# Kernel optimization log

Hardware: AMD Instinct MI355X
Metric: run time of the kernel (lower is better)

The kernel has to match this reference:

```python
import jax, jax.numpy as jnp
import numpy as np

B, L, H, E, V, Z, T = 256, 2, 1024, 256, 28, 1024, 512
SOS_IDX, EOS_IDX = 1, 0


def setup_inputs() -> dict:
    key = jax.random.key(0)
    ks = jax.random.split(key, 16)
    s = 0.05
    emb = s * jax.random.normal(ks[0], (V, E), jnp.float32)
    emb = emb.at[EOS_IDX].set(0.0)  # padding_idx=0
    return {
        "z": jax.random.normal(ks[1], (B, Z), jnp.float32),
        "emb": emb,
        "w_zh": s * jax.random.normal(ks[2], (L * H, Z), jnp.float32),
        "b_zh": jnp.zeros((L * H,), jnp.float32),
        "w_ih0": s * jax.random.normal(ks[3], (3 * H, E), jnp.float32),
        "w_hh0": s * jax.random.normal(ks[4], (3 * H, H), jnp.float32),
        "b_ih0": jnp.zeros((3 * H,), jnp.float32),
        "b_hh0": jnp.zeros((3 * H,), jnp.float32),
        "w_ih1": s * jax.random.normal(ks[5], (3 * H, H), jnp.float32),
        "w_hh1": s * jax.random.normal(ks[6], (3 * H, H), jnp.float32),
        "b_ih1": jnp.zeros((3 * H,), jnp.float32),
        "b_hh1": jnp.zeros((3 * H,), jnp.float32),
        "w_out": s * jax.random.normal(ks[7], (V, H), jnp.float32),
        "b_out": jnp.zeros((V,), jnp.float32),
    }


def _gru_cell(x, h, w_ih, w_hh, b_ih, b_hh):
    # PyTorch GRU cell math
    gi = x @ w_ih.T + b_ih          # [B, 3H]
    gh = h @ w_hh.T + b_hh          # [B, 3H]
    i_r, i_z, i_n = jnp.split(gi, 3, axis=-1)
    h_r, h_z, h_n = jnp.split(gh, 3, axis=-1)
    r = jax.nn.sigmoid(i_r + h_r)
    zg = jax.nn.sigmoid(i_z + h_z)
    n = jnp.tanh(i_n + r * h_n)
    return (1.0 - zg) * n + zg * h


def reference(z, emb, w_zh, b_zh, w_ih0, w_hh0, b_ih0, b_hh0,
              w_ih1, w_hh1, b_ih1, b_hh1, w_out, b_out):
    # init hidden from latent: (B, L*H) -> per-layer (B, H)
    h = jnp.tanh(z @ w_zh.T + b_zh).reshape(-1, L, H)
    h0, h1 = h[:, 0, :], h[:, 1, :]
    tok0 = jnp.full((z.shape[0],), SOS_IDX, jnp.int32)
    keys = jax.random.split(jax.random.key(42), T)

    def step(carry, k):
        tok, h0, h1 = carry
        x = emb[tok]                         # [B, E] embedding lookup
        h0n = _gru_cell(x, h0, w_ih0, w_hh0, b_ih0, b_hh0)
        h1n = _gru_cell(h0n, h1, w_ih1, w_hh1, b_ih1, b_hh1)
        logit = h1n @ w_out.T + b_out        # [B, V]
        tok_n = jax.random.categorical(k, logit)  # multinomial(softmax(logit))
        return (tok_n, h0n, h1n), (logit, tok_n)

    _, (logits, tokens) = jax.lax.scan(step, (tok0, h0, h1), keys)
    # [T, B, V] -> [B, T, V]; [T, B] -> [B, T]
    return logits.transpose(1, 0, 2), tokens.T
```

## Files before the change

kernel.cpp:

```cpp
#include <hip/hip_runtime.h>

#define BB 256
#define HH 1024
#define EE 256
#define VV 28
#define ZZ 1024
#define TT 512
#define G3 3072
#define NTHR 256
#define TOKBASE (BB * TT * VV)

#define BM 64
#define BN 64
#define KT 32

#define MMN 48
#define NBN 64

typedef float f4 __attribute__((ext_vector_type(4)));
typedef float f32x4 __attribute__((ext_vector_type(4)));
typedef _Float16 f16x8 __attribute__((ext_vector_type(8)));
typedef unsigned short u16x4 __attribute__((ext_vector_type(4)));
typedef unsigned short u16x8 __attribute__((ext_vector_type(8)));

#define RES_SCALE 512.0f
#define INV_RES (1.0f / 512.0f)

__device__ __align__(16) float g_h0[2][BB][HH];
__device__ __align__(16) float g_h1[2][BB][HH];
__device__ __align__(16) float g_gh0b[BB][G3];
__device__ __align__(16) float g_gh1b[BB][G3];
__device__ __align__(16) float g_gi1[BB][G3];
__device__ __align__(16) float g_P0[VV][G3];
__device__ __align__(16) unsigned short g_h0t[32][2][4][BB][8];
__device__ __align__(16) unsigned short g_h1t[32][2][4][BB][8];
__device__ __align__(16) unsigned short g_wt[3][NBN][32][2][4][MMN][8];

__device__ __forceinline__ uint2 tf2x32(unsigned k0, unsigned k1,
                                        unsigned x0, unsigned x1) {
  unsigned ks2 = k0 ^ k1 ^ 0x1BD11BDAu;
  unsigned ksl[3] = {k0, k1, ks2};
  x0 += k0; x1 += k1;
#pragma unroll
  for (int g = 0; g < 5; ++g) {
    const int r0 = (g & 1) ? 17 : 13;
    const int r1 = (g & 1) ? 29 : 15;
    const int r2 = (g & 1) ? 16 : 26;
    const int r3 = (g & 1) ? 24 : 6;
    x0 += x1; x1 = (x1 << r0) | (x1 >> (32 - r0)); x1 ^= x0;
    x0 += x1; x1 = (x1 << r1) | (x1 >> (32 - r1)); x1 ^= x0;
    x0 += x1; x1 = (x1 << r2) | (x1 >> (32 - r2)); x1 ^= x0;
    x0 += x1; x1 = (x1 << r3) | (x1 >> (32 - r3)); x1 ^= x0;
    x0 += ksl[(g + 1) % 3];
    x1 += ksl[(g + 2) % 3] + (unsigned)(g + 1);
  }
  return make_uint2(x0, x1);
}

__device__ __forceinline__ float sigf(float x) {
  return 1.0f / (1.0f + expf(-x));
}

__device__ __forceinline__ float gru_h(float i_r, float h_r, float i_z, float h_z,
                                       float i_n, float h_n, float hprev) {
  float r  = sigf(i_r + h_r);
  float zg = sigf(i_z + h_z);
  float n  = tanhf(i_n + r * h_n);
  return (1.0f - zg) * n + zg * hprev;
}

__device__ __forceinline__ void split2(float x, unsigned short& a,
                                       unsigned short& b) {
  _Float16 h1 = (_Float16)x;
  _Float16 h2 = (_Float16)((x - (float)h1) * RES_SCALE);
  a = __builtin_bit_cast(unsigned short, h1);
  b = __builtin_bit_cast(unsigned short, h2);
}

__device__ __forceinline__ void gload16(unsigned short* l, const unsigned short* g) {
  __builtin_amdgcn_global_load_lds(
      (const __attribute__((address_space(1))) unsigned int*)(g),
      (__attribute__((address_space(3))) unsigned int*)(l), 16, 0, 0);
}

__device__ __forceinline__ void gemm_unit(
    const float* __restrict__ At, int lda, int rows_valid,
    const float* __restrict__ Wt, int ldw,
    const float* __restrict__ bias,
    float* __restrict__ Ct, int ldc,
    int K, int mode,
    float (&As)[BM][KT + 4], float (&Ws)[KT][BN + 4]) {
  const int tid = threadIdx.x;
  const int tx = tid & 15, ty = tid >> 4;
  f4 acc0 = {0.f, 0.f, 0.f, 0.f};
  f4 acc1 = {0.f, 0.f, 0.f, 0.f};
  f4 acc2 = {0.f, 0.f, 0.f, 0.f};
  f4 acc3 = {0.f, 0.f, 0.f, 0.f};

  for (int kb = 0; kb < K; kb += KT) {
#pragma unroll
    for (int l = 0; l < 2; ++l) {
      int f = tid + l * NTHR;
      int r = f >> 3, kq = (f & 7) << 2;
      f4 v = {0.f, 0.f, 0.f, 0.f};
      if (r < rows_valid) v = *(const f4*)(At + r * lda + kb + kq);
      *(f4*)&As[r][kq] = v;
    }
#pragma unroll
    for (int l = 0; l < 2; ++l) {
      int f = tid + l * NTHR;
      int nr = f >> 3, kq = (f & 7) << 2;
      f4 v = *(const f4*)(Wt + nr * ldw + kb + kq);
      Ws[kq + 0][nr] = v[0];
      Ws[kq + 1][nr] = v[1];
      Ws[kq + 2][nr] = v[2];
      Ws[kq + 3][nr] = v[3];
    }
    __syncthreads();
#pragma unroll
    for (int kk = 0; kk < KT; kk += 4) {
      f4 a0 = *(const f4*)&As[(ty << 2) + 0][kk];
      f4 a1 = *(const f4*)&As[(ty << 2) + 1][kk];
      f4 a2 = *(const f4*)&As[(ty << 2) + 2][kk];
      f4 a3 = *(const f4*)&As[(ty << 2) + 3][kk];
      f4 b0 = *(const f4*)&Ws[kk + 0][tx << 2];
      f4 b1 = *(const f4*)&Ws[kk + 1][tx << 2];
      f4 b2 = *(const f4*)&Ws[kk + 2][tx << 2];
      f4 b3 = *(const f4*)&Ws[kk + 3][tx << 2];
      acc0 += b0 * a0[0]; acc0 += b1 * a0[1]; acc0 += b2 * a0[2]; acc0 += b3 * a0[3];
      acc1 += b0 * a1[0]; acc1 += b1 * a1[1]; acc1 += b2 * a1[2]; acc1 += b3 * a1[3];
      acc2 += b0 * a2[0]; acc2 += b1 * a2[1]; acc2 += b2 * a2[2]; acc2 += b3 * a2[3];
      acc3 += b0 * a3[0]; acc3 += b1 * a3[1]; acc3 += b2 * a3[2]; acc3 += b3 * a3[3];
    }
    __syncthreads();
  }

  f4 accs[4] = {acc0, acc1, acc2, acc3};
#pragma unroll
  for (int i = 0; i < 4; ++i) {
    int r = (ty << 2) + i;
    if (r < rows_valid) {
#pragma unroll
      for (int j = 0; j < 4; ++j) {
        int c = (tx << 2) + j;
        float v = accs[i][j] + bias[c];
        if (mode == 1) v = tanhf(v);
        Ct[r * ldc + c] = v;
      }
    }
  }
}

#define A_CH (2 * 4 * 128)
#define W_CH (2 * 4 * MMN)
#define BUFSZ ((A_CH + W_CH) * 8)

__device__ __forceinline__ void mm_tile(
    const unsigned short* __restrict__ At,
    const unsigned short* __restrict__ Wt,
    const float* __restrict__ bias,
    float* __restrict__ C,
    int m0, int n0, unsigned short* lds) {
  const int tid = threadIdx.x;
  const int wr = tid >> 6, lane = tid & 63;
  const int lr = lane & 15, lk8 = lane >> 4;

  f32x4 acc1[2][3] = {};
  f32x4 accR[2][3] = {};

  auto stage = [&](int buf, int ks) {
    unsigned short* lA = lds + buf * BUFSZ;
    unsigned short* lW = lA + A_CH * 8;
    const unsigned short* abase = At + (size_t)ks * (2 * 4 * BB * 8);
#pragma unroll
    for (int r = 0; r < 4; ++r) {
      int j = r * NTHR + tid;
      int skk = j >> 7, row = j & 127;
      gload16(lA + j * 8, abase + ((size_t)skk * BB + m0 + row) * 8);
    }
    const unsigned short* wbase = Wt + (size_t)ks * (W_CH * 8);
    gload16(lW + tid * 8, wbase + (size_t)tid * 8);
    if (tid < W_CH - NTHR) {
      int j = NTHR + tid;
      gload16(lW + j * 8, wbase + (size_t)j * 8);
    }
  };

  stage(0, 0);
  int cur = 0;
  for (int ks = 0; ks < HH / 32; ++ks) {
    __syncthreads();
    if (ks + 1 < HH / 32) stage(cur ^ 1, ks + 1);
    const unsigned short* lA = lds + cur * BUFSZ;
    const unsigned short* lW = lA + A_CH * 8;
    f16x8 a[2][2], b[3][2];
#pragma unroll
    for (int mi = 0; mi < 2; ++mi)
#pragma unroll
      for (int s = 0; s < 2; ++s)
        a[mi][s] = *(const f16x8*)(lA + (((s << 2) | lk8) * 128 + wr * 32 + mi * 16 + lr) * 8);
#pragma unroll
    for (int ni = 0; ni < 3; ++ni)
#pragma unroll
      for (int s = 0; s < 2; ++s)
        b[ni][s] = *(const f16x8*)(lW + (((s << 2) | lk8) * MMN + ni * 16 + lr) * 8);
#pragma unroll
    for (int mi = 0; mi < 2; ++mi)
#pragma unroll
      for (int ni = 0; ni < 3; ++ni) {
        acc1[mi][ni] = __builtin_amdgcn_mfma_f32_16x16x32_f16(a[mi][0], b[ni][0], acc1[mi][ni], 0, 0, 0);
        accR[mi][ni] = __builtin_amdgcn_mfma_f32_16x16x32_f16(a[mi][0], b[ni][1], accR[mi][ni], 0, 0, 0);
        accR[mi][ni] = __builtin_amdgcn_mfma_f32_16x16x32_f16(a[mi][1], b[ni][0], accR[mi][ni], 0, 0, 0);
      }
    cur ^= 1;
  }

#pragma unroll
  for (int mi = 0; mi < 2; ++mi) {
    int rowb = m0 + wr * 32 + mi * 16 + ((lane >> 4) << 2);
#pragma unroll
    for (int ni = 0; ni < 3; ++ni) {
      int col = n0 + ni * 16 + lr;
      float bv = bias[col];
#pragma unroll
      for (int r = 0; r < 4; ++r)
        C[(size_t)(rowb + r) * G3 + col] = acc1[mi][ni][r] + accR[mi][ni][r] * INV_RES + bv;
    }
  }
}

__device__ __forceinline__ void write_ht(unsigned short (*ht)[2][4][BB][8],
                                         int row, int k0,
                                         u16x4 o1, u16x4 o2) {
  const int ks = k0 >> 5, kk = (k0 >> 3) & 3, e0 = k0 & 7;
  *(u16x4*)&ht[ks][0][kk][row][e0] = o1;
  *(u16x4*)&ht[ks][1][kk][row][e0] = o2;
}

__global__ __launch_bounds__(NTHR) void k_setup1(
    const float* __restrict__ z, const float* __restrict__ w_zh,
    const float* __restrict__ b_zh, const float* __restrict__ emb,
    const float* __restrict__ w_ih0, const float* __restrict__ b_ih0) {
  __shared__ __align__(16) float As[BM][KT + 4];
  __shared__ __align__(16) float Ws[KT][BN + 4];
  const int bid = blockIdx.x;
  if (bid < 128) {
    int m0 = (bid >> 5) * BM;
    int n0 = (bid & 31) * BN;
    float* Cb;
    int col;
    if (n0 < HH) { Cb = &g_h0[1][0][0]; col = n0; }
    else         { Cb = &g_h1[1][0][0]; col = n0 - HH; }
    gemm_unit(z + m0 * ZZ, ZZ, BM, w_zh + n0 * ZZ, ZZ, b_zh + n0,
              Cb + m0 * HH + col, HH, ZZ, 1, As, Ws);
  } else {
    int n0 = (bid - 128) * BN;
    gemm_unit(emb, EE, VV, w_ih0 + n0 * EE, EE, b_ih0 + n0,
              &g_P0[0][0] + n0, G3, EE, 0, As, Ws);
  }
}

__global__ __launch_bounds__(NTHR) void k_splitw(
    const float* __restrict__ w_ih1, const float* __restrict__ w_hh0,
    const float* __restrict__ w_hh1) {
  unsigned u = blockIdx.x * NTHR + threadIdx.x;
  int row = u % MMN;
  unsigned v = u / MMN;
  int kk = v & 3, ks = (v >> 2) & 31;
  unsigned rem = v >> 7;
  int mat = rem / NBN, bn = rem % NBN;
  const float* src = (mat == 0) ? w_ih1 : (mat == 1) ? w_hh0 : w_hh1;
  const float* p = src + (size_t)(bn * MMN + row) * HH + ks * 32 + kk * 8;
  f4 v0 = *(const f4*)p;
  f4 v1 = *(const f4*)(p + 4);
  u16x8 o1, o2;
#pragma unroll
  for (int c = 0; c < 8; ++c) {
    float x = (c < 4) ? v0[c] : v1[c - 4];
    unsigned short a, b;
    split2(x, a, b);
    o1[c] = a; o2[c] = b;
  }
  *(u16x8*)&g_wt[mat][bn][ks][0][kk][row][0] = o1;
  *(u16x8*)&g_wt[mat][bn][ks][1][kk][row][0] = o2;
}

__global__ __launch_bounds__(NTHR) void k_splith() {
  unsigned e = blockIdx.x * NTHR + threadIdx.x;
  int mat = e >> 16, r = (e >> 8) & 255, k0 = (e & 255) << 2;
  const float* src = (mat == 0) ? &g_h0[1][0][0] : &g_h1[1][0][0];
  f4 v = *(const f4*)(src + (size_t)r * HH + k0);
  u16x4 o1, o2;
#pragma unroll
  for (int c = 0; c < 4; ++c) {
    unsigned short a, b;
    split2(v[c], a, b);
    o1[c] = a; o2[c] = b;
  }
  write_ht((mat == 0) ? g_h0t : g_h1t, r, k0, o1, o2);
}

__global__ __launch_bounds__(NTHR, 3) void k_mm_init(const float* __restrict__ b_hh0) {
  __shared__ __align__(16) unsigned short lds[2 * BUFSZ];
  int mt = blockIdx.x >> 6, bn = blockIdx.x & 63;
  mm_tile(&g_h0t[0][0][0][0][0], &g_wt[1][bn][0][0][0][0][0], b_hh0,
          &g_gh0b[0][0], mt * 128, bn * MMN, lds);
}

__global__ __launch_bounds__(NTHR) void k_gate0_init() {
  const int b = blockIdx.x, tid = threadIdx.x, j = tid << 2;
  const float* __restrict__ gi = g_P0[1];
  const float* __restrict__ gh = g_gh0b[b];
  f4 ir = *(const f4*)&gi[j];
  f4 iz = *(const f4*)&gi[j + HH];
  f4 in_ = *(const f4*)&gi[j + 2 * HH];
  f4 hr = *(const f4*)&gh[j];
  f4 hz = *(const f4*)&gh[j + HH];
  f4 hn = *(const f4*)&gh[j + 2 * HH];
  f4 hp = *(const f4*)&g_h0[1][b][j];
  f4 ho;
  u16x4 o1, o2;
#pragma unroll
  for (int c = 0; c < 4; ++c) {
    ho[c] = gru_h(ir[c], hr[c], iz[c], hz[c], in_[c], hn[c], hp[c]);
    unsigned short a, bb2;
    split2(ho[c], a, bb2);
    o1[c] = a; o2[c] = bb2;
  }
  *(f4*)&g_h0[0][b][j] = ho;
  write_ht(g_h0t, b, j, o1, o2);
}

__global__ __launch_bounds__(NTHR, 3) void k_mm(
    const float* __restrict__ b_ih1, const float* __restrict__ b_hh0,
    const float* __restrict__ b_hh1) {
  __shared__ __align__(16) unsigned short lds[2 * BUFSZ];
  const int bid = blockIdx.x;
  const int mt = bid / 192, r = bid % 192;
  const int mat = r >> 6, bn = r & 63;
  const unsigned short* At = (mat == 2) ? &g_h1t[0][0][0][0][0] : &g_h0t[0][0][0][0][0];
  const unsigned short* Wt = &g_wt[mat][bn][0][0][0][0][0];
  const float* bias = (mat == 0) ? b_ih1 : (mat == 1) ? b_hh0 : b_hh1;
  float* C = (mat == 0) ? &g_gi1[0][0] : (mat == 1) ? &g_gh0b[0][0] : &g_gh1b[0][0];
  mm_tile(At, Wt, bias, C, mt * 128, bn * MMN, lds);
}

__global__ __launch_bounds__(NTHR) void k_fuse(
    int t, const float* __restrict__ w_out, const float* __restrict__ b_out,
    float* __restrict__ out) {
  __shared__ __align__(16) float s_h[HH];
  __shared__ float s_log[32];
  __shared__ float s_score[32];
  __shared__ int s_tok;
  const int b = blockIdx.x, tid = threadIdx.x, j = tid << 2;
  const int pw = t & 1, pr = pw ^ 1;

  {
    const float* __restrict__ gi = g_gi1[b];
    const float* __restrict__ gh = g_gh1b[b];
    f4 ir = *(const f4*)&gi[j];
    f4 iz = *(const f4*)&gi[j + HH];
    f4 in_ = *(const f4*)&gi[j + 2 * HH];
    f4 hr = *(const f4*)&gh[j];
    f4 hz = *(const f4*)&gh[j + HH];
    f4 hn = *(const f4*)&gh[j + 2 * HH];
    f4 hp = *(const f4*)&g_h1[pr][b][j];
    f4 ho;
    u16x4 o1, o2;
#pragma unroll
    for (int c = 0; c < 4; ++c) {
      ho[c] = gru_h(ir[c], hr[c], iz[c], hz[c], in_[c], hn[c], hp[c]);
      unsigned short a, bb2;
      split2(ho[c], a, bb2);
      o1[c] = a; o2[c] = bb2;
    }
    *(f4*)&g_h1[pw][b][j] = ho;
    *(f4*)&s_h[j] = ho;
    write_ht(g_h1t, b, j, o1, o2);
  }
  __syncthreads();

  {
    const int v = tid >> 3, ks = tid & 7;
    float part = 0.f;
    if (v < VV) {
      const float* __restrict__ wrow = w_out + v * HH + ks * 128;
      const float* __restrict__ hh = s_h + ks * 128;
#pragma unroll 8
      for (int i = 0; i < 128; i += 4) {
        f4 wv = *(const f4*)&wrow[i];
        f4 hv = *(const f4*)&hh[i];
        part += hv[0] * wv[0] + hv[1] * wv[1] + hv[2] * wv[2] + hv[3] * wv[3];
      }
    }
    part += __shfl_xor(part, 1);
    part += __shfl_xor(part, 2);
    part += __shfl_xor(part, 4);
    if (v < VV && ks == 0) s_log[v] = part;
  }
  __syncthreads();

  if (tid < VV) {
    float logit = s_log[tid] + b_out[tid];
    out[(size_t)b * (TT * VV) + (size_t)t * VV + tid] = logit;
    uint2 kt = tf2x32(0u, 42u, 0u, (unsigned)t);
    uint2 rr = tf2x32(kt.x, kt.y, 0u, (unsigned)(b * VV + tid));
    unsigned bits = rr.x ^ rr.y;
    float uf = __uint_as_float((bits >> 9) | 0x3f800000u) - 1.0f;
    if (uf <= 0.0f) uf = 1.17549435e-38f;
    s_score[tid] = logit - logf(-logf(uf));
  }
  __syncthreads();
  if (tid == 0) {
    float best = s_score[0];
    int bv = 0;
    for (int vv = 1; vv < VV; ++vv) {
      float s = s_score[vv];
      if (s > best) { best = s; bv = vv; }
    }
    s_tok = bv;
    out[TOKBASE + (size_t)b * TT + t] = (float)bv;
  }
  __syncthreads();

  {
    const int tok = s_tok;
    const float* __restrict__ gi = g_P0[tok];
    const float* __restrict__ gh = g_gh0b[b];
    f4 ir = *(const f4*)&gi[j];
    f4 iz = *(const f4*)&gi[j + HH];
    f4 in_ = *(const f4*)&gi[j + 2 * HH];
    f4 hr = *(const f4*)&gh[j];
    f4 hz = *(const f4*)&gh[j + HH];
    f4 hn = *(const f4*)&gh[j + 2 * HH];
    f4 hp = *(const f4*)&g_h0[pw][b][j];
    f4 ho;
    u16x4 o1, o2;
#pragma unroll
    for (int c = 0; c < 4; ++c) {
      ho[c] = gru_h(ir[c], hr[c], iz[c], hz[c], in_[c], hn[c], hp[c]);
      unsigned short a, bb2;
      split2(ho[c], a, bb2);
      o1[c] = a; o2[c] = bb2;
    }
    *(f4*)&g_h0[pr][b][j] = ho;
    write_ht(g_h0t, b, j, o1, o2);
  }
}

extern "C" void kernel_launch(void* const* d_in, const int* in_sizes, int n_in,
                              void* d_out, int out_size, void* d_ws, size_t ws_size,
                              hipStream_t stream) {
  (void)in_sizes; (void)n_in; (void)d_ws; (void)ws_size; (void)out_size;
  const float* z     = (const float*)d_in[0];
  const float* emb   = (const float*)d_in[1];
  const float* w_zh  = (const float*)d_in[2];
  const float* b_zh  = (const float*)d_in[3];
  const float* w_ih0 = (const float*)d_in[4];
  const float* w_hh0 = (const float*)d_in[5];
  const float* b_ih0 = (const float*)d_in[6];
  const float* b_hh0 = (const float*)d_in[7];
  const float* w_ih1 = (const float*)d_in[8];
  const float* w_hh1 = (const float*)d_in[9];
  const float* b_ih1 = (const float*)d_in[10];
  const float* b_hh1 = (const float*)d_in[11];
  const float* w_out = (const float*)d_in[12];
  const float* b_out = (const float*)d_in[13];
  float* out = (float*)d_out;

  k_setup1<<<dim3(176), dim3(NTHR), 0, stream>>>(z, w_zh, b_zh, emb, w_ih0, b_ih0);
  k_splitw<<<dim3(4608), dim3(NTHR), 0, stream>>>(w_ih1, w_hh0, w_hh1);
  k_splith<<<dim3(512), dim3(NTHR), 0, stream>>>();
  k_mm_init<<<dim3(128), dim3(NTHR), 0, stream>>>(b_hh0);
  k_gate0_init<<<dim3(BB), dim3(NTHR), 0, stream>>>();

  for (int t = 0; t < TT; ++t) {
    k_mm<<<dim3(384), dim3(NTHR), 0, stream>>>(b_ih1, b_hh0, b_hh1);
    k_fuse<<<dim3(BB), dim3(NTHR), 0, stream>>>(t, w_out, b_out, out);
  }
}
```

Before: 15.99 ms.

## Load A fragments directly from global into registers, stage only W in LDS

```diff
diff --git a/kernel.cpp b/kernel.cpp
--- a/kernel.cpp
+++ b/kernel.cpp
@@ -151,9 +151,9 @@
   }
 }
 
-#define A_CH (2 * 4 * 128)
 #define W_CH (2 * 4 * MMN)
-#define BUFSZ ((A_CH + W_CH) * 8)
+#define WBUF (W_CH * 8)
+#define A_KS_STRIDE (2 * 4 * BB * 8)
 
 __device__ __forceinline__ void mm_tile(
     const unsigned short* __restrict__ At,
@@ -168,17 +168,11 @@
   f32x4 acc1[2][3] = {};
   f32x4 accR[2][3] = {};
 
-  auto stage = [&](int buf, int ks) {
-    unsigned short* lA = lds + buf * BUFSZ;
-    unsigned short* lW = lA + A_CH * 8;
-    const unsigned short* abase = At + (size_t)ks * (2 * 4 * BB * 8);
-#pragma unroll
-    for (int r = 0; r < 4; ++r) {
-      int j = r * NTHR + tid;
-      int skk = j >> 7, row = j & 127;
-      gload16(lA + j * 8, abase + ((size_t)skk * BB + m0 + row) * 8);
-    }
-    const unsigned short* wbase = Wt + (size_t)ks * (W_CH * 8);
+  const unsigned short* abase = At + ((size_t)lk8 * BB + m0 + wr * 32 + lr) * 8;
+
+  auto stageW = [&](int buf, int ks) {
+    unsigned short* lW = lds + buf * WBUF;
+    const unsigned short* wbase = Wt + (size_t)ks * WBUF;
     gload16(lW + tid * 8, wbase + (size_t)tid * 8);
     if (tid < W_CH - NTHR) {
       int j = NTHR + tid;
@@ -186,19 +180,18 @@
     }
   };
 
-  stage(0, 0);
-  int cur = 0;
-  for (int ks = 0; ks < HH / 32; ++ks) {
-    __syncthreads();
-    if (ks + 1 < HH / 32) stage(cur ^ 1, ks + 1);
-    const unsigned short* lA = lds + cur * BUFSZ;
-    const unsigned short* lW = lA + A_CH * 8;
-    f16x8 a[2][2], b[3][2];
+  auto loadA = [&](int ks, f16x8 (&a)[2][2]) {
 #pragma unroll
     for (int mi = 0; mi < 2; ++mi)
 #pragma unroll
       for (int s = 0; s < 2; ++s)
-        a[mi][s] = *(const f16x8*)(lA + (((s << 2) | lk8) * 128 + wr * 32 + mi * 16 + lr) * 8);
+        a[mi][s] = *(const f16x8*)(abase + (size_t)ks * A_KS_STRIDE +
+                                   ((size_t)s * 4 * BB + mi * 16) * 8);
+  };
+
+  auto compute = [&](int buf, f16x8 (&a)[2][2]) {
+    const unsigned short* lW = lds + buf * WBUF;
+    f16x8 b[3][2];
 #pragma unroll
     for (int ni = 0; ni < 3; ++ni)
 #pragma unroll
@@ -212,7 +205,22 @@
         accR[mi][ni] = __builtin_amdgcn_mfma_f32_16x16x32_f16(a[mi][0], b[ni][1], accR[mi][ni], 0, 0, 0);
         accR[mi][ni] = __builtin_amdgcn_mfma_f32_16x16x32_f16(a[mi][1], b[ni][0], accR[mi][ni], 0, 0, 0);
       }
-    cur ^= 1;
+  };
+
+  f16x8 aA[2][2], aB[2][2];
+  stageW(0, 0);
+  loadA(0, aA);
+  for (int kp = 0; kp < 16; ++kp) {
+    __syncthreads();
+    stageW(1, 2 * kp + 1);
+    loadA(2 * kp + 1, aB);
+    compute(0, aA);
+    __syncthreads();
+    if (kp < 15) {
+      stageW(0, 2 * kp + 2);
+      loadA(2 * kp + 2, aA);
+    }
+    compute(1, aB);
   }
 
 #pragma unroll
@@ -301,7 +309,7 @@
 }
 
 __global__ __launch_bounds__(NTHR, 3) void k_mm_init(const float* __restrict__ b_hh0) {
-  __shared__ __align__(16) unsigned short lds[2 * BUFSZ];
+  __shared__ __align__(16) unsigned short lds[2 * WBUF];
   int mt = blockIdx.x >> 6, bn = blockIdx.x & 63;
   mm_tile(&g_h0t[0][0][0][0][0], &g_wt[1][bn][0][0][0][0][0], b_hh0,
           &g_gh0b[0][0], mt * 128, bn * MMN, lds);
@@ -334,7 +342,7 @@
 __global__ __launch_bounds__(NTHR, 3) void k_mm(
     const float* __restrict__ b_ih1, const float* __restrict__ b_hh0,
     const float* __restrict__ b_hh1) {
-  __shared__ __align__(16) unsigned short lds[2 * BUFSZ];
+  __shared__ __align__(16) unsigned short lds[2 * WBUF];
   const int bid = blockIdx.x;
   const int mt = bid / 192, r = bid % 192;
   const int mat = r >> 6, bn = r & 63;
```

After: 17.71 ms. +10.7%, slower.

## Triple-buffer LDS in GEMM tile with explicit vmcnt waits and MFMA priority

Applied to the files above, without the earlier changes.

```diff
diff --git a/kernel.cpp b/kernel.cpp
--- a/kernel.cpp
+++ b/kernel.cpp
@@ -164,13 +164,14 @@
   const int tid = threadIdx.x;
   const int wr = tid >> 6, lane = tid & 63;
   const int lr = lane & 15, lk8 = lane >> 4;
+  const bool hiW = (tid < 128);
 
   f32x4 acc1[2][3] = {};
   f32x4 accR[2][3] = {};
 
-  auto stage = [&](int buf, int ks) {
-    unsigned short* lA = lds + buf * BUFSZ;
-    unsigned short* lW = lA + A_CH * 8;
+  auto stage = [&](unsigned short* lbuf, int ks) {
+    unsigned short* lA = lbuf;
+    unsigned short* lW = lbuf + A_CH * 8;
     const unsigned short* abase = At + (size_t)ks * (2 * 4 * BB * 8);
 #pragma unroll
     for (int r = 0; r < 4; ++r) {
@@ -186,13 +187,9 @@
     }
   };
 
-  stage(0, 0);
-  int cur = 0;
-  for (int ks = 0; ks < HH / 32; ++ks) {
-    __syncthreads();
-    if (ks + 1 < HH / 32) stage(cur ^ 1, ks + 1);
-    const unsigned short* lA = lds + cur * BUFSZ;
-    const unsigned short* lW = lA + A_CH * 8;
+  auto compute = [&](const unsigned short* lbuf) {
+    const unsigned short* lA = lbuf;
+    const unsigned short* lW = lbuf + A_CH * 8;
     f16x8 a[2][2], b[3][2];
 #pragma unroll
     for (int mi = 0; mi < 2; ++mi)
@@ -204,6 +201,7 @@
 #pragma unroll
       for (int s = 0; s < 2; ++s)
         b[ni][s] = *(const f16x8*)(lW + (((s << 2) | lk8) * MMN + ni * 16 + lr) * 8);
+    __builtin_amdgcn_s_setprio(1);
 #pragma unroll
     for (int mi = 0; mi < 2; ++mi)
 #pragma unroll
@@ -212,7 +210,21 @@
         accR[mi][ni] = __builtin_amdgcn_mfma_f32_16x16x32_f16(a[mi][0], b[ni][1], accR[mi][ni], 0, 0, 0);
         accR[mi][ni] = __builtin_amdgcn_mfma_f32_16x16x32_f16(a[mi][1], b[ni][0], accR[mi][ni], 0, 0, 0);
       }
-    cur ^= 1;
+    __builtin_amdgcn_s_setprio(0);
+  };
+
+  stage(lds, 0);
+  stage(lds + BUFSZ, 1);
+  for (int ks = 0; ks < 32; ++ks) {
+    if (ks < 31) {
+      if (hiW) asm volatile("s_waitcnt vmcnt(6)" ::: "memory");
+      else     asm volatile("s_waitcnt vmcnt(5)" ::: "memory");
+    } else {
+      asm volatile("s_waitcnt vmcnt(0)" ::: "memory");
+    }
+    __builtin_amdgcn_s_barrier();
+    compute(lds + (ks % 3) * BUFSZ);
+    if (ks + 2 < 32) stage(lds + ((ks + 2) % 3) * BUFSZ, ks + 2);
   }
 
 #pragma unroll
@@ -300,8 +312,8 @@
   write_ht((mat == 0) ? g_h0t : g_h1t, r, k0, o1, o2);
 }
 
-__global__ __launch_bounds__(NTHR, 3) void k_mm_init(const float* __restrict__ b_hh0) {
-  __shared__ __align__(16) unsigned short lds[2 * BUFSZ];
+__global__ __launch_bounds__(NTHR, 2) void k_mm_init(const float* __restrict__ b_hh0) {
+  __shared__ __align__(16) unsigned short lds[3 * BUFSZ];
   int mt = blockIdx.x >> 6, bn = blockIdx.x & 63;
   mm_tile(&g_h0t[0][0][0][0][0], &g_wt[1][bn][0][0][0][0][0], b_hh0,
           &g_gh0b[0][0], mt * 128, bn * MMN, lds);
@@ -331,10 +343,10 @@
   write_ht(g_h0t, b, j, o1, o2);
 }
 
-__global__ __launch_bounds__(NTHR, 3) void k_mm(
+__global__ __launch_bounds__(NTHR, 2) void k_mm(
     const float* __restrict__ b_ih1, const float* __restrict__ b_hh0,
     const float* __restrict__ b_hh1) {
-  __shared__ __align__(16) unsigned short lds[2 * BUFSZ];
+  __shared__ __align__(16) unsigned short lds[3 * BUFSZ];
   const int bid = blockIdx.x;
   const int mt = bid / 192, r = bid % 192;
   const int mat = r >> 6, bn = r & 63;
```

After: 15.96 ms, median of 2. About the same (-0.2%).
